# Kernel tuning notes

Measured on AMD Instinct MI355X. Metric: run time of the kernel, lower is better.

Reference implementation:

```python
import jax, jax.numpy as jnp
import numpy as np

E = 8          # n_routed_experts
TOP_K = 2      # num_experts_per_tok
H = 1024       # hidden_size
I = 512        # moe_intermediate_size
SI = 512       # shared expert intermediate (I * n_shared_experts)
B, S = 4, 4096


def setup_inputs() -> dict:
    key = jax.random.key(0)
    ks = jax.random.split(key, 8)
    sc_h = 1.0 / np.sqrt(H)
    sc_i = 1.0 / np.sqrt(I)
    return {
        "hidden_states": jax.random.normal(ks[0], (B, S, H), jnp.float32),
        "gate_w": jax.random.normal(ks[1], (E, H), jnp.float32) * sc_h,  # router logits weight [E,H]
        "Wg": jax.random.normal(ks[2], (E, H, I), jnp.float32) * sc_h,   # per-expert gate_proj
        "Wu": jax.random.normal(ks[3], (E, H, I), jnp.float32) * sc_h,   # per-expert up_proj
        "Wd": jax.random.normal(ks[4], (E, I, H), jnp.float32) * sc_i,   # per-expert down_proj
        "sWg": jax.random.normal(ks[5], (H, SI), jnp.float32) * sc_h,    # shared expert gate_proj
        "sWu": jax.random.normal(ks[6], (H, SI), jnp.float32) * sc_h,
        "sWd": jax.random.normal(ks[7], (SI, H), jnp.float32) * sc_i,
    }


def reference(hidden_states, gate_w, Wg, Wu, Wd, sWg, sWu, sWd):
    b, s, h = hidden_states.shape
    x = hidden_states.reshape(-1, h)                      # [T,H]

    # ---- MoEGate: softmax scoring + greedy top-k + weight normalization ----
    logits = x.astype(jnp.float32) @ gate_w.T             # [T,E]
    scores = jax.nn.softmax(logits, axis=-1)
    topk_w, topk_idx = jax.lax.top_k(scores, TOP_K)       # [T,K]
    topk_w = topk_w / (topk_w.sum(-1, keepdims=True) + 1e-20)  # norm_topk_prob

    # combine weights as a dense [T,E] map (scatter of topk weights)
    cw = (jax.nn.one_hot(topk_idx, E, dtype=topk_w.dtype) * topk_w[..., None]).sum(1)  # [T,E]

    # ---- routed experts: down(gelu(gate(x)) * up(x)), combined by gate weight ----
    g = jnp.einsum("th,ehi->tei", x, Wg)
    u = jnp.einsum("th,ehi->tei", x, Wu)
    inter = jax.nn.gelu(g, approximate=False) * u         # [T,E,I]
    y = jnp.einsum("tei,te,eih->th", inter, cw.astype(x.dtype), Wd)

    # ---- shared expert on the identity path ----
    sh = (jax.nn.gelu(x @ sWg, approximate=False) * (x @ sWu)) @ sWd

    return (y + sh).reshape(b, s, h)
```

## Files before the change

kernel.cpp:

```cpp
#include <hip/hip_runtime.h>
#include <hip/hip_bf16.h>
#include <math.h>


#define T_TOTAL 16384
#define HDIM 1024
#define IDIM 512
#define NE 9
#define CNT_STRIDE 16

typedef __bf16 bf16x8 __attribute__((ext_vector_type(8)));
typedef float f32x4 __attribute__((ext_vector_type(4)));

typedef __attribute__((address_space(1))) void gvoid_t;
typedef __attribute__((address_space(3))) void lvoid_t;

__device__ __forceinline__ void load_lds16(const void* g, void* l) {
  __builtin_amdgcn_global_load_lds((const gvoid_t*)g, (lvoid_t*)l, 16, 0, 0);
}

__device__ __forceinline__ f32x4 mfma_bf16(bf16x8 a, bf16x8 b, f32x4 c) {
  return __builtin_amdgcn_mfma_f32_16x16x32_bf16(a, b, c, 0, 0, 0);
}

__global__ __launch_bounds__(256) void k_gate(const float* __restrict__ x,
                                              const float* __restrict__ gw,
                                              __bf16* __restrict__ xb,
                                              int* __restrict__ tok,
                                              float* __restrict__ wtl,
                                              int* __restrict__ cnt,
                                              int* __restrict__ inv) {
  __shared__ int s_eid[64][2];
  __shared__ float s_wt[64][2];
  __shared__ int s_rank[64][2];
  __shared__ int lcnt[8];
  __shared__ int lbase[8];
  const int wv = threadIdx.x >> 6, lane = threadIdx.x & 63;
  if (threadIdx.x < 8) lcnt[threadIdx.x] = 0;
  __syncthreads();

  for (int i = 0; i < 16; i++) {
    const int tl = wv * 16 + i;
    const int t = blockIdx.x * 64 + tl;
    const float* xr = x + (size_t)t * HDIM + lane * 16;
    float4 xv[4];
#pragma unroll
    for (int j = 0; j < 4; j++) xv[j] = ((const float4*)xr)[j];

    bf16x8 v0, v1;
#pragma unroll
    for (int j = 0; j < 8; j++) v0[j] = (__bf16)((const float*)xv)[j];
#pragma unroll
    for (int j = 0; j < 8; j++) v1[j] = (__bf16)((const float*)xv)[j + 8];
    bf16x8* xbo = (bf16x8*)(xb + (size_t)t * HDIM + lane * 16);
    xbo[0] = v0;
    xbo[1] = v1;

    float acc[8];
#pragma unroll
    for (int e = 0; e < 8; e++) {
      const float4* gp = (const float4*)(gw + e * HDIM + lane * 16);
      float s = 0.f;
#pragma unroll
      for (int j = 0; j < 4; j++) {
        float4 g = gp[j];
        s += xv[j].x * g.x + xv[j].y * g.y + xv[j].z * g.z + xv[j].w * g.w;
      }
      acc[e] = s;
    }
#pragma unroll
    for (int d = 32; d >= 1; d >>= 1) {
#pragma unroll
      for (int e = 0; e < 8; e++) acc[e] += __shfl_xor(acc[e], d, 64);
    }
    if (lane == 0) {
      float mx = acc[0];
#pragma unroll
      for (int e = 1; e < 8; e++) mx = fmaxf(mx, acc[e]);
      float p[8], Z = 0.f;
#pragma unroll
      for (int e = 0; e < 8; e++) {
        p[e] = expf(acc[e] - mx);
        Z += p[e];
      }
#pragma unroll
      for (int e = 0; e < 8; e++) p[e] /= Z;
      int i1 = 0;
#pragma unroll
      for (int e = 1; e < 8; e++)
        if (p[e] > p[i1]) i1 = e;
      int i2 = (i1 == 0) ? 1 : 0;
#pragma unroll
      for (int e = 0; e < 8; e++)
        if (e != i1 && p[e] > p[i2]) i2 = e;
      const float s12 = p[i1] + p[i2] + 1e-20f;
      s_eid[tl][0] = i1;
      s_eid[tl][1] = i2;
      s_wt[tl][0] = p[i1] / s12;
      s_wt[tl][1] = p[i2] / s12;
    }
  }
  __syncthreads();

  if (threadIdx.x < 64) {
    s_rank[threadIdx.x][0] = atomicAdd(&lcnt[s_eid[threadIdx.x][0]], 1);
    s_rank[threadIdx.x][1] = atomicAdd(&lcnt[s_eid[threadIdx.x][1]], 1);
  }
  __syncthreads();
  if (threadIdx.x < 8)
    lbase[threadIdx.x] =
        atomicAdd(&cnt[threadIdx.x * CNT_STRIDE], lcnt[threadIdx.x]);
  __syncthreads();
  if (threadIdx.x < 64) {
    const int t = blockIdx.x * 64 + threadIdx.x;
#pragma unroll
    for (int j = 0; j < 2; j++) {
      const int e = s_eid[threadIdx.x][j];
      const int slot = lbase[e] + s_rank[threadIdx.x][j];
      tok[e * T_TOTAL + slot] = t;
      wtl[e * T_TOTAL + slot] = s_wt[threadIdx.x][j];
      inv[t * 2 + j] = e * T_TOTAL + slot;
    }
  }
}

__global__ void k_scan(const int* __restrict__ cnt, int* __restrict__ base) {
  if (threadIdx.x == 0 && blockIdx.x == 0) {
    int s = 0;
#pragma unroll
    for (int e = 0; e < 8; e++) {
      base[e] = s;
      s += cnt[e * CNT_STRIDE];
    }
  }
}

__global__ __launch_bounds__(256) void k_transpose(const float* __restrict__ w8,
                                                   const float* __restrict__ w1,
                                                   __bf16* __restrict__ out,
                                                   int R, int C) {
  __shared__ float tile[32][33];
  const int b = blockIdx.z;
  const float* src = (b < 8) ? (w8 + (size_t)b * R * C) : w1;
  const int c0 = blockIdx.x * 32, r0 = blockIdx.y * 32;
  const int tx = threadIdx.x & 31, ty = threadIdx.x >> 5;
#pragma unroll
  for (int i = 0; i < 4; i++)
    tile[ty + i * 8][tx] = src[(size_t)(r0 + ty + i * 8) * C + c0 + tx];
  __syncthreads();
#pragma unroll
  for (int i = 0; i < 4; i++)
    out[(size_t)b * R * C + (size_t)(c0 + ty + i * 8) * R + r0 + tx] =
        (__bf16)tile[tx][ty + i * 8];
}

__global__ __launch_bounds__(256) void k_transpose_fuse(
    const float* __restrict__ w8, const float* __restrict__ w1,
    __bf16* __restrict__ out, int u16off) {
  __shared__ float tile[32][33];
  const int b = blockIdx.z;
  const float* src = (b < 8) ? (w8 + (size_t)b * HDIM * IDIM) : w1;
  const int c0 = blockIdx.x * 32, r0 = blockIdx.y * 32;
  const int tx = threadIdx.x & 31, ty = threadIdx.x >> 5;
#pragma unroll
  for (int i = 0; i < 4; i++)
    tile[ty + i * 8][tx] = src[(size_t)(r0 + ty + i * 8) * IDIM + c0 + tx];
  __syncthreads();
#pragma unroll
  for (int i = 0; i < 4; i++) {
    const int ic = c0 + ty + i * 8;
    const int f = 2 * (ic & ~15) + (ic & 15) + u16off;
    out[(size_t)b * 1024 * HDIM + (size_t)f * HDIM + r0 + tx] =
        (__bf16)tile[tx][ty + i * 8];
  }
}

__global__ __launch_bounds__(256, 2) void k_gu(
    const __bf16* __restrict__ xb, const __bf16* __restrict__ Wfu,
    const int* __restrict__ tok, const float* __restrict__ wtl,
    const int* __restrict__ cnt, __bf16* __restrict__ inter) {
  const int e = blockIdx.z;
  const bool se = (e == 8);
  const int cnt_e = se ? T_TOTAL : cnt[e * CNT_STRIDE];
  const int m0 = blockIdx.x * 128;
  if (m0 >= cnt_e) return;

  __shared__ __bf16 sA[128][64];
  __shared__ __bf16 sB[128][64];
  const int tid = threadIdx.x, w = tid >> 6, lane = tid & 63;
  const int n0 = blockIdx.y * 128;
  const int quad = lane >> 4, l16 = lane & 15;
  const int wm = (w & 1) * 64, wn = (w >> 1) * 64;

  const int sr = tid >> 3;
  const int scs = ((tid & 7) ^ (sr & 7)) * 8;
  const __bf16* ap[4];
  const __bf16* bp[4];
#pragma unroll
  for (int sh = 0; sh < 4; sh++) {
    int s = m0 + sh * 32 + sr;
    if (s > cnt_e - 1) s = cnt_e - 1;
    const int t = se ? s : tok[e * T_TOTAL + s];
    ap[sh] = xb + (size_t)t * HDIM + scs;
    bp[sh] = Wfu + ((size_t)e * 1024 + n0 + sh * 32 + sr) * HDIM + scs;
  }
  char* const la = (char*)sA + w * 1024;
  char* const lb = (char*)sB + w * 1024;

  f32x4 acc[4][4];
#pragma unroll
  for (int im = 0; im < 4; im++)
#pragma unroll
    for (int in = 0; in < 4; in++) acc[im][in] = {0.f, 0.f, 0.f, 0.f};

  for (int k = 0; k < HDIM; k += 64) {
    __syncthreads();
#pragma unroll
    for (int sh = 0; sh < 4; sh++) {
      load_lds16(ap[sh], la + sh * 4096);
      load_lds16(bp[sh], lb + sh * 4096);
      ap[sh] += 64;
      bp[sh] += 64;
    }
    __syncthreads();
#pragma unroll
    for (int kh = 0; kh < 2; kh++) {
      bf16x8 af[4], bfr[4];
#pragma unroll
      for (int i = 0; i < 4; i++) {
        const int ra = wm + i * 16 + l16;
        af[i] = *(const bf16x8*)((const char*)sA + ra * 128 +
                                 ((kh * 4 + quad) ^ (ra & 7)) * 16);
        const int rb = wn + i * 16 + l16;
        bfr[i] = *(const bf16x8*)((const char*)sB + rb * 128 +
                                  ((kh * 4 + quad) ^ (rb & 7)) * 16);
      }
#pragma unroll
      for (int im = 0; im < 4; im++)
#pragma unroll
        for (int in = 0; in < 4; in++)
          acc[im][in] = mfma_bf16(af[im], bfr[in], acc[im][in]);
    }
  }

#pragma unroll
  for (int im = 0; im < 4; im++) {
#pragma unroll
    for (int r = 0; r < 4; r++) {
      const int slot = m0 + wm + im * 16 + quad * 4 + r;
      if (slot < cnt_e) {
        const float wt = se ? 1.0f : wtl[e * T_TOTAL + slot];
        __bf16* op =
            inter + ((size_t)e * T_TOTAL + slot) * IDIM + ((n0 + wn) >> 1) + l16;
#pragma unroll
        for (int p = 0; p < 2; p++) {
          const float g = acc[im][2 * p][r];
          const float u = acc[im][2 * p + 1][r];
          const float v =
              wt * u * 0.5f * g * (1.0f + erff(g * 0.70710678118654752f));
          op[p * 16] = (__bf16)v;
        }
      }
    }
  }
}

__global__ __launch_bounds__(256, 2) void k_down_s(const __bf16* __restrict__ iA,
                                                   const __bf16* __restrict__ wB,
                                                   float* __restrict__ out) {
  __shared__ __bf16 sA[128][64];
  __shared__ __bf16 sB[128][64];
  const int tid = threadIdx.x, w = tid >> 6, lane = tid & 63;
  const int m0 = blockIdx.x * 128, n0 = blockIdx.y * 128;
  const int quad = lane >> 4, l16 = lane & 15;
  const int wm = (w & 1) * 64, wn = (w >> 1) * 64;

  const int sr = tid >> 3;
  const int scs = ((tid & 7) ^ (sr & 7)) * 8;
  const __bf16* ap[4];
  const __bf16* bp[4];
#pragma unroll
  for (int sh = 0; sh < 4; sh++) {
    ap[sh] = iA + (size_t)(m0 + sh * 32 + sr) * IDIM + scs;
    bp[sh] = wB + (size_t)(n0 + sh * 32 + sr) * IDIM + scs;
  }
  char* const la = (char*)sA + w * 1024;
  char* const lb = (char*)sB + w * 1024;

  f32x4 acc[4][4];
#pragma unroll
  for (int im = 0; im < 4; im++)
#pragma unroll
    for (int in = 0; in < 4; in++) acc[im][in] = {0.f, 0.f, 0.f, 0.f};

  for (int k = 0; k < IDIM; k += 64) {
    __syncthreads();
#pragma unroll
    for (int sh = 0; sh < 4; sh++) {
      load_lds16(ap[sh], la + sh * 4096);
      load_lds16(bp[sh], lb + sh * 4096);
      ap[sh] += 64;
      bp[sh] += 64;
    }
    __syncthreads();
#pragma unroll
    for (int kh = 0; kh < 2; kh++) {
      bf16x8 af[4], bfr[4];
#pragma unroll
      for (int i = 0; i < 4; i++) {
        const int ra = wm + i * 16 + l16;
        af[i] = *(const bf16x8*)((const char*)sA + ra * 128 +
                                 ((kh * 4 + quad) ^ (ra & 7)) * 16);
        const int rb = wn + i * 16 + l16;
        bfr[i] = *(const bf16x8*)((const char*)sB + rb * 128 +
                                  ((kh * 4 + quad) ^ (rb & 7)) * 16);
      }
#pragma unroll
      for (int im = 0; im < 4; im++)
#pragma unroll
        for (int in = 0; in < 4; in++)
          acc[im][in] = mfma_bf16(af[im], bfr[in], acc[im][in]);
    }
  }

#pragma unroll
  for (int im = 0; im < 4; im++) {
#pragma unroll
    for (int r = 0; r < 4; r++) {
      const int t = m0 + wm + im * 16 + quad * 4 + r;
#pragma unroll
      for (int in = 0; in < 4; in++)
        out[(size_t)t * HDIM + n0 + wn + in * 16 + l16] = acc[im][in][r];
    }
  }
}

__global__ __launch_bounds__(256, 2) void k_down_rs(
    const __bf16* __restrict__ inter, const __bf16* __restrict__ WdT,
    const int* __restrict__ cnt, const int* __restrict__ base,
    float* __restrict__ yb) {
  const int e = blockIdx.z;
  const int cnt_e = cnt[e * CNT_STRIDE];
  const int m0 = blockIdx.x * 128;
  if (m0 >= cnt_e) return;
  const int rowb = base[e];

  __shared__ __bf16 sA[128][64];
  __shared__ __bf16 sB[128][64];
  const int tid = threadIdx.x, w = tid >> 6, lane = tid & 63;
  const int n0 = blockIdx.y * 128;
  const int quad = lane >> 4, l16 = lane & 15;
  const int wm = (w & 1) * 64, wn = (w >> 1) * 64;

  const int sr = tid >> 3;
  const int scs = ((tid & 7) ^ (sr & 7)) * 8;
  const __bf16* ap[4];
  const __bf16* bp[4];
#pragma unroll
  for (int sh = 0; sh < 4; sh++) {
    int s = m0 + sh * 32 + sr;
    if (s > cnt_e - 1) s = cnt_e - 1;
    ap[sh] = inter + ((size_t)e * T_TOTAL + s) * IDIM + scs;
    bp[sh] = WdT + ((size_t)e * HDIM + n0 + sh * 32 + sr) * IDIM + scs;
  }
  char* const la = (char*)sA + w * 1024;
  char* const lb = (char*)sB + w * 1024;

  f32x4 acc[4][4];
#pragma unroll
  for (int im = 0; im < 4; im++)
#pragma unroll
    for (int in = 0; in < 4; in++) acc[im][in] = {0.f, 0.f, 0.f, 0.f};

  for (int k = 0; k < IDIM; k += 64) {
    __syncthreads();
#pragma unroll
    for (int sh = 0; sh < 4; sh++) {
      load_lds16(ap[sh], la + sh * 4096);
      load_lds16(bp[sh], lb + sh * 4096);
      ap[sh] += 64;
      bp[sh] += 64;
    }
    __syncthreads();
#pragma unroll
    for (int kh = 0; kh < 2; kh++) {
      bf16x8 af[4], bfr[4];
#pragma unroll
      for (int i = 0; i < 4; i++) {
        const int ra = wm + i * 16 + l16;
        af[i] = *(const bf16x8*)((const char*)sA + ra * 128 +
                                 ((kh * 4 + quad) ^ (ra & 7)) * 16);
        const int rb = wn + i * 16 + l16;
        bfr[i] = *(const bf16x8*)((const char*)sB + rb * 128 +
                                  ((kh * 4 + quad) ^ (rb & 7)) * 16);
      }
#pragma unroll
      for (int im = 0; im < 4; im++)
#pragma unroll
        for (int in = 0; in < 4; in++)
          acc[im][in] = mfma_bf16(af[im], bfr[in], acc[im][in]);
    }
  }

#pragma unroll
  for (int im = 0; im < 4; im++) {
#pragma unroll
    for (int r = 0; r < 4; r++) {
      const int slot = m0 + wm + im * 16 + quad * 4 + r;
      if (slot < cnt_e) {
        float* op = yb + (size_t)(rowb + slot) * HDIM + n0 + wn + l16;
#pragma unroll
        for (int in = 0; in < 4; in++) op[in * 16] = acc[im][in][r];
      }
    }
  }
}

__global__ __launch_bounds__(256) void k_combine(const float* __restrict__ yb,
                                                 const int* __restrict__ inv,
                                                 const int* __restrict__ base,
                                                 float* __restrict__ out) {
  const int t = blockIdx.x * 4 + (threadIdx.x >> 6);
  const int lane = threadIdx.x & 63;
  const int v1 = inv[2 * t], v2 = inv[2 * t + 1];
  const int r1 = base[v1 >> 14] + (v1 & (T_TOTAL - 1));
  const int r2 = base[v2 >> 14] + (v2 & (T_TOTAL - 1));
  const float4* y1 = (const float4*)(yb + (size_t)r1 * HDIM);
  const float4* y2 = (const float4*)(yb + (size_t)r2 * HDIM);
  float4* o = (float4*)(out + (size_t)t * HDIM);
#pragma unroll
  for (int j = 0; j < 4; j++) {
    const int c = lane + j * 64;
    float4 a = o[c];
    float4 b = y1[c];
    float4 d = y2[c];
    o[c] = make_float4(a.x + b.x + d.x, a.y + b.y + d.y, a.z + b.z + d.z,
                       a.w + b.w + d.w);
  }
}

__global__ __launch_bounds__(256, 2) void k_down_r(
    const __bf16* __restrict__ inter, const __bf16* __restrict__ WdT,
    const int* __restrict__ tok, const int* __restrict__ cnt,
    float* __restrict__ out) {
  const int e = blockIdx.z;
  const int cnt_e = cnt[e * CNT_STRIDE];
  const int m0 = blockIdx.x * 128;
  if (m0 >= cnt_e) return;

  __shared__ __bf16 sA[128][64];
  __shared__ __bf16 sB[128][64];
  const int tid = threadIdx.x, w = tid >> 6, lane = tid & 63;
  const int n0 = blockIdx.y * 128;
  const int quad = lane >> 4, l16 = lane & 15;
  const int wm = (w & 1) * 64, wn = (w >> 1) * 64;

  const int sr = tid >> 3;
  const int scs = ((tid & 7) ^ (sr & 7)) * 8;
  const __bf16* ap[4];
  const __bf16* bp[4];
#pragma unroll
  for (int sh = 0; sh < 4; sh++) {
    int s = m0 + sh * 32 + sr;
    if (s > cnt_e - 1) s = cnt_e - 1;
    ap[sh] = inter + ((size_t)e * T_TOTAL + s) * IDIM + scs;
    bp[sh] = WdT + ((size_t)e * HDIM + n0 + sh * 32 + sr) * IDIM + scs;
  }
  char* const la = (char*)sA + w * 1024;
  char* const lb = (char*)sB + w * 1024;

  f32x4 acc[4][4];
#pragma unroll
  for (int im = 0; im < 4; im++)
#pragma unroll
    for (int in = 0; in < 4; in++) acc[im][in] = {0.f, 0.f, 0.f, 0.f};

  for (int k = 0; k < IDIM; k += 64) {
    __syncthreads();
#pragma unroll
    for (int sh = 0; sh < 4; sh++) {
      load_lds16(ap[sh], la + sh * 4096);
      load_lds16(bp[sh], lb + sh * 4096);
      ap[sh] += 64;
      bp[sh] += 64;
    }
    __syncthreads();
#pragma unroll
    for (int kh = 0; kh < 2; kh++) {
      bf16x8 af[4], bfr[4];
#pragma unroll
      for (int i = 0; i < 4; i++) {
        const int ra = wm + i * 16 + l16;
        af[i] = *(const bf16x8*)((const char*)sA + ra * 128 +
                                 ((kh * 4 + quad) ^ (ra & 7)) * 16);
        const int rb = wn + i * 16 + l16;
        bfr[i] = *(const bf16x8*)((const char*)sB + rb * 128 +
                                  ((kh * 4 + quad) ^ (rb & 7)) * 16);
      }
#pragma unroll
      for (int im = 0; im < 4; im++)
#pragma unroll
        for (int in = 0; in < 4; in++)
          acc[im][in] = mfma_bf16(af[im], bfr[in], acc[im][in]);
    }
  }

#pragma unroll
  for (int im = 0; im < 4; im++) {
#pragma unroll
    for (int r = 0; r < 4; r++) {
      const int slot = m0 + wm + im * 16 + quad * 4 + r;
      if (slot < cnt_e) {
        const int t = tok[e * T_TOTAL + slot];
#pragma unroll
        for (int in = 0; in < 4; in++)
          atomicAdd(&out[(size_t)t * HDIM + n0 + wn + in * 16 + l16],
                    acc[im][in][r]);
      }
    }
  }
}

extern "C" void kernel_launch(void* const* d_in, const int* in_sizes, int n_in,
                              void* d_out, int out_size, void* d_ws,
                              size_t ws_size, hipStream_t stream) {
  const float* x = (const float*)d_in[0];
  const float* gw = (const float*)d_in[1];
  const float* Wg = (const float*)d_in[2];
  const float* Wu = (const float*)d_in[3];
  const float* Wd = (const float*)d_in[4];
  const float* sWg = (const float*)d_in[5];
  const float* sWu = (const float*)d_in[6];
  const float* sWd = (const float*)d_in[7];
  float* out = (float*)d_out;

  char* ws = (char*)d_ws;
  size_t off = 0;
  auto alloc = [&](size_t n) {
    char* p = ws + off;
    off += (n + 255) & ~(size_t)255;
    return p;
  };
  __bf16* xb = (__bf16*)alloc((size_t)T_TOTAL * HDIM * 2);
  __bf16* Wfu = (__bf16*)alloc((size_t)NE * 1024 * HDIM * 2);
  __bf16* WdT = (__bf16*)alloc((size_t)NE * HDIM * IDIM * 2);
  int* tok = (int*)alloc((size_t)8 * T_TOTAL * 4);
  float* wtl = (float*)alloc((size_t)8 * T_TOTAL * 4);
  int* cnt = (int*)alloc(8 * CNT_STRIDE * 4);
  int* inv = (int*)alloc((size_t)T_TOTAL * 2 * 4);
  int* base = (int*)alloc(16 * 4);
  __bf16* inter = (__bf16*)alloc((size_t)NE * T_TOTAL * IDIM * 2);

  const size_t yb_bytes = (size_t)2 * T_TOTAL * HDIM * 4;
  const bool store_path = (off + yb_bytes) <= ws_size;
  float* yb = store_path ? (float*)alloc(yb_bytes) : nullptr;

  hipMemsetAsync(cnt, 0, 8 * CNT_STRIDE * 4, stream);

  k_gate<<<dim3(T_TOTAL / 64), dim3(256), 0, stream>>>(x, gw, xb, tok, wtl,
                                                       cnt, inv);
  k_transpose_fuse<<<dim3(IDIM / 32, HDIM / 32, NE), dim3(256), 0, stream>>>(
      Wg, sWg, Wfu, 0);
  k_transpose_fuse<<<dim3(IDIM / 32, HDIM / 32, NE), dim3(256), 0, stream>>>(
      Wu, sWu, Wfu, 16);
  k_transpose<<<dim3(HDIM / 32, IDIM / 32, NE), dim3(256), 0, stream>>>(
      Wd, sWd, WdT, IDIM, HDIM);
  k_scan<<<dim3(1), dim3(64), 0, stream>>>(cnt, base);

  k_gu<<<dim3(T_TOTAL / 128, 1024 / 128, NE), dim3(256), 0, stream>>>(
      xb, Wfu, tok, wtl, cnt, inter);

  k_down_s<<<dim3(T_TOTAL / 128, HDIM / 128), dim3(256), 0, stream>>>(
      inter + (size_t)8 * T_TOTAL * IDIM, WdT + (size_t)8 * HDIM * IDIM, out);

  if (store_path) {
    k_down_rs<<<dim3(T_TOTAL / 128, HDIM / 128, 8), dim3(256), 0, stream>>>(
        inter, WdT, cnt, base, yb);
    k_combine<<<dim3(T_TOTAL / 4), dim3(256), 0, stream>>>(yb, inv, base, out);
  } else {
    k_down_r<<<dim3(T_TOTAL / 128, HDIM / 128, 8), dim3(256), 0, stream>>>(
        inter, WdT, tok, cnt, out);
  }
}
```

Measured before the change: 501.0 us.

## Fuse combine into shared-expert down GEMM and widen weight transposes

The separate combine kernel is removed. The shared-expert down-projection epilogue now adds the two routed-expert rows from the staging buffer and writes the final output once, saving a full read-modify-write pass over the output. Weight transposes move to 64x64 tiles with float4 loads and 16-byte bf16x8 stores to cut global transaction count. The gate/up kernel is split into routed and shared launches, which adds a launch and some scattered reads in the GEMM epilogue.

Result: no change. 493.6 us (-1.5%).

```diff
diff --git a/kernel.cpp b/kernel.cpp
--- a/kernel.cpp
+++ b/kernel.cpp
@@ -135,51 +135,78 @@
   }
 }
 
-__global__ __launch_bounds__(256) void k_transpose(const float* __restrict__ w8,
-                                                   const float* __restrict__ w1,
-                                                   __bf16* __restrict__ out,
-                                                   int R, int C) {
-  __shared__ float tile[32][33];
+__global__ __launch_bounds__(256) void k_transpose64(
+    const float* __restrict__ w8, const float* __restrict__ w1,
+    __bf16* __restrict__ out) {
+  __shared__ float tile[64][65];
   const int b = blockIdx.z;
-  const float* src = (b < 8) ? (w8 + (size_t)b * R * C) : w1;
-  const int c0 = blockIdx.x * 32, r0 = blockIdx.y * 32;
-  const int tx = threadIdx.x & 31, ty = threadIdx.x >> 5;
-#pragma unroll
-  for (int i = 0; i < 4; i++)
-    tile[ty + i * 8][tx] = src[(size_t)(r0 + ty + i * 8) * C + c0 + tx];
+  const float* src = (b < 8) ? (w8 + (size_t)b * IDIM * HDIM) : w1;
+  const int c0 = blockIdx.x * 64, r0 = blockIdx.y * 64;
+  const int t = threadIdx.x;
+
+#pragma unroll
+  for (int j = 0; j < 4; j++) {
+    const int rr = (t >> 4) + j * 16;
+    const int cc = (t & 15) * 4;
+    const float4 v = *(const float4*)(src + (size_t)(r0 + rr) * HDIM + c0 + cc);
+    tile[rr][cc] = v.x;
+    tile[rr][cc + 1] = v.y;
+    tile[rr][cc + 2] = v.z;
+    tile[rr][cc + 3] = v.w;
+  }
   __syncthreads();
-#pragma unroll
-  for (int i = 0; i < 4; i++)
-    out[(size_t)b * R * C + (size_t)(c0 + ty + i * 8) * R + r0 + tx] =
-        (__bf16)tile[tx][ty + i * 8];
-}
-
-__global__ __launch_bounds__(256) void k_transpose_fuse(
+
+#pragma unroll
+  for (int j = 0; j < 2; j++) {
+    const int cidx = (t >> 3) + j * 32;
+    const int rseg = (t & 7) * 8;
+    bf16x8 v;
+#pragma unroll
+    for (int k = 0; k < 8; k++) v[k] = (__bf16)tile[rseg + k][cidx];
+    *(bf16x8*)(out + (size_t)b * HDIM * IDIM + (size_t)(c0 + cidx) * IDIM + r0 +
+               rseg) = v;
+  }
+}
+
+__global__ __launch_bounds__(256) void k_transpose_fuse64(
     const float* __restrict__ w8, const float* __restrict__ w1,
     __bf16* __restrict__ out, int u16off) {
-  __shared__ float tile[32][33];
+  __shared__ float tile[64][65];
   const int b = blockIdx.z;
   const float* src = (b < 8) ? (w8 + (size_t)b * HDIM * IDIM) : w1;
-  const int c0 = blockIdx.x * 32, r0 = blockIdx.y * 32;
-  const int tx = threadIdx.x & 31, ty = threadIdx.x >> 5;
-#pragma unroll
-  for (int i = 0; i < 4; i++)
-    tile[ty + i * 8][tx] = src[(size_t)(r0 + ty + i * 8) * IDIM + c0 + tx];
+  const int c0 = blockIdx.x * 64, r0 = blockIdx.y * 64;
+  const int t = threadIdx.x;
+
+#pragma unroll
+  for (int j = 0; j < 4; j++) {
+    const int rr = (t >> 4) + j * 16;
+    const int cc = (t & 15) * 4;
+    const float4 v = *(const float4*)(src + (size_t)(r0 + rr) * IDIM + c0 + cc);
+    tile[rr][cc] = v.x;
+    tile[rr][cc + 1] = v.y;
+    tile[rr][cc + 2] = v.z;
+    tile[rr][cc + 3] = v.w;
+  }
   __syncthreads();
-#pragma unroll
-  for (int i = 0; i < 4; i++) {
-    const int ic = c0 + ty + i * 8;
+
+#pragma unroll
+  for (int j = 0; j < 2; j++) {
+    const int cidx = (t >> 3) + j * 32;
+    const int rseg = (t & 7) * 8;
+    const int ic = c0 + cidx;
     const int f = 2 * (ic & ~15) + (ic & 15) + u16off;
-    out[(size_t)b * 1024 * HDIM + (size_t)f * HDIM + r0 + tx] =
-        (__bf16)tile[tx][ty + i * 8];
+    bf16x8 v;
+#pragma unroll
+    for (int k = 0; k < 8; k++) v[k] = (__bf16)tile[rseg + k][cidx];
+    *(bf16x8*)(out + (size_t)b * 1024 * HDIM + (size_t)f * HDIM + r0 + rseg) = v;
   }
 }
 
 __global__ __launch_bounds__(256, 2) void k_gu(
     const __bf16* __restrict__ xb, const __bf16* __restrict__ Wfu,
     const int* __restrict__ tok, const float* __restrict__ wtl,
-    const int* __restrict__ cnt, __bf16* __restrict__ inter) {
-  const int e = blockIdx.z;
+    const int* __restrict__ cnt, __bf16* __restrict__ inter, int zbase) {
+  const int e = blockIdx.z + zbase;
   const bool se = (e == 8);
   const int cnt_e = se ? T_TOTAL : cnt[e * CNT_STRIDE];
   const int m0 = blockIdx.x * 128;
@@ -261,6 +288,164 @@
           op[p * 16] = (__bf16)v;
         }
       }
+    }
+  }
+}
+
+__global__ __launch_bounds__(256, 2) void k_down_rs(
+    const __bf16* __restrict__ inter, const __bf16* __restrict__ WdT,
+    const int* __restrict__ cnt, const int* __restrict__ base,
+    float* __restrict__ yb) {
+  const int e = blockIdx.z;
+  const int cnt_e = cnt[e * CNT_STRIDE];
+  const int m0 = blockIdx.x * 128;
+  if (m0 >= cnt_e) return;
+  const int rowb = base[e];
+
+  __shared__ __bf16 sA[128][64];
+  __shared__ __bf16 sB[128][64];
+  const int tid = threadIdx.x, w = tid >> 6, lane = tid & 63;
+  const int n0 = blockIdx.y * 128;
+  const int quad = lane >> 4, l16 = lane & 15;
+  const int wm = (w & 1) * 64, wn = (w >> 1) * 64;
+
+  const int sr = tid >> 3;
+  const int scs = ((tid & 7) ^ (sr & 7)) * 8;
+  const __bf16* ap[4];
+  const __bf16* bp[4];
+#pragma unroll
+  for (int sh = 0; sh < 4; sh++) {
+    int s = m0 + sh * 32 + sr;
+    if (s > cnt_e - 1) s = cnt_e - 1;
+    ap[sh] = inter + ((size_t)e * T_TOTAL + s) * IDIM + scs;
+    bp[sh] = WdT + ((size_t)e * HDIM + n0 + sh * 32 + sr) * IDIM + scs;
+  }
+  char* const la = (char*)sA + w * 1024;
+  char* const lb = (char*)sB + w * 1024;
+
+  f32x4 acc[4][4];
+#pragma unroll
+  for (int im = 0; im < 4; im++)
+#pragma unroll
+    for (int in = 0; in < 4; in++) acc[im][in] = {0.f, 0.f, 0.f, 0.f};
+
+  for (int k = 0; k < IDIM; k += 64) {
+    __syncthreads();
+#pragma unroll
+    for (int sh = 0; sh < 4; sh++) {
+      load_lds16(ap[sh], la + sh * 4096);
+      load_lds16(bp[sh], lb + sh * 4096);
+      ap[sh] += 64;
+      bp[sh] += 64;
+    }
+    __syncthreads();
+#pragma unroll
+    for (int kh = 0; kh < 2; kh++) {
+      bf16x8 af[4], bfr[4];
+#pragma unroll
+      for (int i = 0; i < 4; i++) {
+        const int ra = wm + i * 16 + l16;
+        af[i] = *(const bf16x8*)((const char*)sA + ra * 128 +
+                                 ((kh * 4 + quad) ^ (ra & 7)) * 16);
+        const int rb = wn + i * 16 + l16;
+        bfr[i] = *(const bf16x8*)((const char*)sB + rb * 128 +
+                                  ((kh * 4 + quad) ^ (rb & 7)) * 16);
+      }
+#pragma unroll
+      for (int im = 0; im < 4; im++)
+#pragma unroll
+        for (int in = 0; in < 4; in++)
+          acc[im][in] = mfma_bf16(af[im], bfr[in], acc[im][in]);
+    }
+  }
+
+#pragma unroll
+  for (int im = 0; im < 4; im++) {
+#pragma unroll
+    for (int r = 0; r < 4; r++) {
+      const int slot = m0 + wm + im * 16 + quad * 4 + r;
+      if (slot < cnt_e) {
+        float* op = yb + (size_t)(rowb + slot) * HDIM + n0 + wn + l16;
+#pragma unroll
+        for (int in = 0; in < 4; in++) op[in * 16] = acc[im][in][r];
+      }
+    }
+  }
+}
+
+__global__ __launch_bounds__(256, 2) void k_down_sc(
+    const __bf16* __restrict__ iA, const __bf16* __restrict__ wB,
+    const float* __restrict__ yb, const int* __restrict__ inv,
+    const int* __restrict__ base, float* __restrict__ out) {
+  __shared__ __bf16 sA[128][64];
+  __shared__ __bf16 sB[128][64];
+  const int tid = threadIdx.x, w = tid >> 6, lane = tid & 63;
+  const int m0 = blockIdx.x * 128, n0 = blockIdx.y * 128;
+  const int quad = lane >> 4, l16 = lane & 15;
+  const int wm = (w & 1) * 64, wn = (w >> 1) * 64;
+
+  const int sr = tid >> 3;
+  const int scs = ((tid & 7) ^ (sr & 7)) * 8;
+  const __bf16* ap[4];
+  const __bf16* bp[4];
+#pragma unroll
+  for (int sh = 0; sh < 4; sh++) {
+    ap[sh] = iA + (size_t)(m0 + sh * 32 + sr) * IDIM + scs;
+    bp[sh] = wB + (size_t)(n0 + sh * 32 + sr) * IDIM + scs;
+  }
+  char* const la = (char*)sA + w * 1024;
+  char* const lb = (char*)sB + w * 1024;
+
+  f32x4 acc[4][4];
+#pragma unroll
+  for (int im = 0; im < 4; im++)
+#pragma unroll
+    for (int in = 0; in < 4; in++) acc[im][in] = {0.f, 0.f, 0.f, 0.f};
+
+  for (int k = 0; k < IDIM; k += 64) {
+    __syncthreads();
+#pragma unroll
+    for (int sh = 0; sh < 4; sh++) {
+      load_lds16(ap[sh], la + sh * 4096);
+      load_lds16(bp[sh], lb + sh * 4096);
+      ap[sh] += 64;
+      bp[sh] += 64;
+    }
+    __syncthreads();
+#pragma unroll
+    for (int kh = 0; kh < 2; kh++) {
+      bf16x8 af[4], bfr[4];
+#pragma unroll
+      for (int i = 0; i < 4; i++) {
+        const int ra = wm + i * 16 + l16;
+        af[i] = *(const bf16x8*)((const char*)sA + ra * 128 +
+                                 ((kh * 4 + quad) ^ (ra & 7)) * 16);
+        const int rb = wn + i * 16 + l16;
+        bfr[i] = *(const bf16x8*)((const char*)sB + rb * 128 +
+                                  ((kh * 4 + quad) ^ (rb & 7)) * 16);
+      }
+#pragma unroll
+      for (int im = 0; im < 4; im++)
+#pragma unroll
+        for (int in = 0; in < 4; in++)
+          acc[im][in] = mfma_bf16(af[im], bfr[in], acc[im][in]);
+    }
+  }
+
+#pragma unroll
+  for (int im = 0; im < 4; im++) {
+#pragma unroll
+    for (int r = 0; r < 4; r++) {
+      const int t = m0 + wm + im * 16 + quad * 4 + r;
+      const int v1 = inv[2 * t], v2 = inv[2 * t + 1];
+      const int r1 = base[v1 >> 14] + (v1 & (T_TOTAL - 1));
+      const int r2 = base[v2 >> 14] + (v2 & (T_TOTAL - 1));
+      const float* y1 = yb + (size_t)r1 * HDIM + n0 + wn + l16;
+      const float* y2 = yb + (size_t)r2 * HDIM + n0 + wn + l16;
+      float* op = out + (size_t)t * HDIM + n0 + wn + l16;
+#pragma unroll
+      for (int in = 0; in < 4; in++)
+        op[in * 16] = acc[im][in][r] + y1[in * 16] + y2[in * 16];
     }
   }
 }
@@ -332,110 +517,6 @@
       for (int in = 0; in < 4; in++)
         out[(size_t)t * HDIM + n0 + wn + in * 16 + l16] = acc[im][in][r];
     }
-  }
-}
-
-__global__ __launch_bounds__(256, 2) void k_down_rs(
-    const __bf16* __restrict__ inter, const __bf16* __restrict__ WdT,
-    const int* __restrict__ cnt, const int* __restrict__ base,
-    float* __restrict__ yb) {
-  const int e = blockIdx.z;
-  const int cnt_e = cnt[e * CNT_STRIDE];
-  const int m0 = blockIdx.x * 128;
-  if (m0 >= cnt_e) return;
-  const int rowb = base[e];
-
-  __shared__ __bf16 sA[128][64];
-  __shared__ __bf16 sB[128][64];
-  const int tid = threadIdx.x, w = tid >> 6, lane = tid & 63;
-  const int n0 = blockIdx.y * 128;
-  const int quad = lane >> 4, l16 = lane & 15;
-  const int wm = (w & 1) * 64, wn = (w >> 1) * 64;
-
-  const int sr = tid >> 3;
-  const int scs = ((tid & 7) ^ (sr & 7)) * 8;
-  const __bf16* ap[4];
-  const __bf16* bp[4];
-#pragma unroll
-  for (int sh = 0; sh < 4; sh++) {
-    int s = m0 + sh * 32 + sr;
-    if (s > cnt_e - 1) s = cnt_e - 1;
-    ap[sh] = inter + ((size_t)e * T_TOTAL + s) * IDIM + scs;
-    bp[sh] = WdT + ((size_t)e * HDIM + n0 + sh * 32 + sr) * IDIM + scs;
-  }
-  char* const la = (char*)sA + w * 1024;
-  char* const lb = (char*)sB + w * 1024;
-
-  f32x4 acc[4][4];
-#pragma unroll
-  for (int im = 0; im < 4; im++)
-#pragma unroll
-    for (int in = 0; in < 4; in++) acc[im][in] = {0.f, 0.f, 0.f, 0.f};
-
-  for (int k = 0; k < IDIM; k += 64) {
-    __syncthreads();
-#pragma unroll
-    for (int sh = 0; sh < 4; sh++) {
-      load_lds16(ap[sh], la + sh * 4096);
-      load_lds16(bp[sh], lb + sh * 4096);
-      ap[sh] += 64;
-      bp[sh] += 64;
-    }
-    __syncthreads();
-#pragma unroll
-    for (int kh = 0; kh < 2; kh++) {
-      bf16x8 af[4], bfr[4];
-#pragma unroll
-      for (int i = 0; i < 4; i++) {
-        const int ra = wm + i * 16 + l16;
-        af[i] = *(const bf16x8*)((const char*)sA + ra * 128 +
-                                 ((kh * 4 + quad) ^ (ra & 7)) * 16);
-        const int rb = wn + i * 16 + l16;
-        bfr[i] = *(const bf16x8*)((const char*)sB + rb * 128 +
-                                  ((kh * 4 + quad) ^ (rb & 7)) * 16);
-      }
-#pragma unroll
-      for (int im = 0; im < 4; im++)
-#pragma unroll
-        for (int in = 0; in < 4; in++)
-          acc[im][in] = mfma_bf16(af[im], bfr[in], acc[im][in]);
-    }
-  }
-
-#pragma unroll
-  for (int im = 0; im < 4; im++) {
-#pragma unroll
-    for (int r = 0; r < 4; r++) {
-      const int slot = m0 + wm + im * 16 + quad * 4 + r;
-      if (slot < cnt_e) {
-        float* op = yb + (size_t)(rowb + slot) * HDIM + n0 + wn + l16;
-#pragma unroll
-        for (int in = 0; in < 4; in++) op[in * 16] = acc[im][in][r];
-      }
-    }
-  }
-}
-
-__global__ __launch_bounds__(256) void k_combine(const float* __restrict__ yb,
-                                                 const int* __restrict__ inv,
-                                                 const int* __restrict__ base,
-                                                 float* __restrict__ out) {
-  const int t = blockIdx.x * 4 + (threadIdx.x >> 6);
-  const int lane = threadIdx.x & 63;
-  const int v1 = inv[2 * t], v2 = inv[2 * t + 1];
-  const int r1 = base[v1 >> 14] + (v1 & (T_TOTAL - 1));
-  const int r2 = base[v2 >> 14] + (v2 & (T_TOTAL - 1));
-  const float4* y1 = (const float4*)(yb + (size_t)r1 * HDIM);
-  const float4* y2 = (const float4*)(yb + (size_t)r2 * HDIM);
-  float4* o = (float4*)(out + (size_t)t * HDIM);
-#pragma unroll
-  for (int j = 0; j < 4; j++) {
-    const int c = lane + j * 64;
-    float4 a = o[c];
-    float4 b = y1[c];
-    float4 d = y2[c];
-    o[c] = make_float4(a.x + b.x + d.x, a.y + b.y + d.y, a.z + b.z + d.z,
-                       a.w + b.w + d.w);
   }
 }
 
@@ -559,25 +640,28 @@
 
   k_gate<<<dim3(T_TOTAL / 64), dim3(256), 0, stream>>>(x, gw, xb, tok, wtl,
                                                        cnt, inv);
-  k_transpose_fuse<<<dim3(IDIM / 32, HDIM / 32, NE), dim3(256), 0, stream>>>(
+  k_transpose_fuse64<<<dim3(IDIM / 64, HDIM / 64, NE), dim3(256), 0, stream>>>(
       Wg, sWg, Wfu, 0);
-  k_transpose_fuse<<<dim3(IDIM / 32, HDIM / 32, NE), dim3(256), 0, stream>>>(
+  k_transpose_fuse64<<<dim3(IDIM / 64, HDIM / 64, NE), dim3(256), 0, stream>>>(
       Wu, sWu, Wfu, 16);
-  k_transpose<<<dim3(HDIM / 32, IDIM / 32, NE), dim3(256), 0, stream>>>(
-      Wd, sWd, WdT, IDIM, HDIM);
+  k_transpose64<<<dim3(HDIM / 64, IDIM / 64, NE), dim3(256), 0, stream>>>(
+      Wd, sWd, WdT);
   k_scan<<<dim3(1), dim3(64), 0, stream>>>(cnt, base);
 
-  k_gu<<<dim3(T_TOTAL / 128, 1024 / 128, NE), dim3(256), 0, stream>>>(
-      xb, Wfu, tok, wtl, cnt, inter);
-
-  k_down_s<<<dim3(T_TOTAL / 128, HDIM / 128), dim3(256), 0, stream>>>(
-      inter + (size_t)8 * T_TOTAL * IDIM, WdT + (size_t)8 * HDIM * IDIM, out);
+  k_gu<<<dim3(T_TOTAL / 128, 1024 / 128, 8), dim3(256), 0, stream>>>(
+      xb, Wfu, tok, wtl, cnt, inter, 0);
+  k_gu<<<dim3(T_TOTAL / 128, 1024 / 128, 1), dim3(256), 0, stream>>>(
+      xb, Wfu, tok, wtl, cnt, inter, 8);
 
   if (store_path) {
     k_down_rs<<<dim3(T_TOTAL / 128, HDIM / 128, 8), dim3(256), 0, stream>>>(
         inter, WdT, cnt, base, yb);
-    k_combine<<<dim3(T_TOTAL / 4), dim3(256), 0, stream>>>(yb, inv, base, out);
+    k_down_sc<<<dim3(T_TOTAL / 128, HDIM / 128), dim3(256), 0, stream>>>(
+        inter + (size_t)8 * T_TOTAL * IDIM, WdT + (size_t)8 * HDIM * IDIM, yb,
+        inv, base, out);
   } else {
+    k_down_s<<<dim3(T_TOTAL / 128, HDIM / 128), dim3(256), 0, stream>>>(
+        inter + (size_t)8 * T_TOTAL * IDIM, WdT + (size_t)8 * HDIM * IDIM, out);
     k_down_r<<<dim3(T_TOTAL / 128, HDIM / 128, 8), dim3(256), 0, stream>>>(
         inter, WdT, tok, cnt, out);
   }
```
